# Kernel optimization log

Measured on AMD Instinct MI355X. Metric: run time of the kernel, lower is better.

Reference implementation:

```python
import jax, jax.numpy as jnp
import numpy as np

NUM_HEADS = 16

def setup_inputs() -> dict:
    key = jax.random.key(0)
    ks = jax.random.split(key, 8)
    T, B, E = 2048, 2, 1024
    s = 1.0 / np.sqrt(E)
    return {
        "query": jax.random.normal(ks[0], (T, B, E), jnp.float32),
        "key": jax.random.normal(ks[1], (T, B, E), jnp.float32),
        "value": jax.random.normal(ks[2], (T, B, E), jnp.float32),
        "Wq": jax.random.normal(ks[3], (E, E), jnp.float32) * s,
        "bq": jnp.zeros((E,), jnp.float32),
        "Wk": jax.random.normal(ks[4], (E, E), jnp.float32) * s,
        "bk": jnp.zeros((E,), jnp.float32),
        "Wv": jax.random.normal(ks[5], (E, E), jnp.float32) * s,
        "bv": jnp.zeros((E,), jnp.float32),
        "Wo": jax.random.normal(ks[6], (E, E), jnp.float32) * s,
        "bo": jnp.zeros((E,), jnp.float32),
    }

def reference(query, key, value, Wq, bq, Wk, bk, Wv, bv, Wo, bo):
    T, B, E = query.shape
    S = key.shape[0]
    H = NUM_HEADS
    hd = E // H
    scaling = float(hd) ** -0.5
    # linear projections (torch Linear: x @ W.T + b)
    q = (query @ Wq.T + bq).reshape(T, B, H, hd)
    k = (key @ Wk.T + bk).reshape(S, B, H, hd)
    v = (value @ Wv.T + bv).reshape(S, B, H, hd)
    # scores: (B, H, T, S)
    scores = jnp.einsum('tbhd,sbhd->bhts', q, k) * scaling
    attn = jax.nn.softmax(scores, axis=-1)  # dropout p=0
    # weighted sum: (T, B, H, hd) -> (T, B, E)
    out = jnp.einsum('bhts,sbhd->tbhd', attn, v).reshape(T, B, E)
    out = out @ Wo.T + bo
    # averaged attention weights over heads: (B, T, S)
    avg_w = attn.mean(axis=1)
    return (out, avg_w)
```

## Files before the change

kernel.cpp:

```cpp
#include <hip/hip_runtime.h>
#include <hip/hip_bf16.h>
#include <stdint.h>

#define HN 16
#define TT 2048
#define BBATCH 2
#define EE 1024
#define HD 64
#define MM 4096

#define SCALEQ 0.18033688011112042f

typedef __attribute__((ext_vector_type(8))) __bf16 bfrag;
typedef __attribute__((ext_vector_type(4))) float f32x4;

struct alignas(8) B4 { __bf16 a0, a1, a2, a3; };

__device__ __forceinline__ void gll16(const void* g, void* lds) {
  __builtin_amdgcn_global_load_lds(
      (const __attribute__((address_space(1))) void*)g,
      (__attribute__((address_space(3))) void*)lds, 16, 0, 0);
}

__device__ __forceinline__ f32x4 mfma_bf16(bfrag a, bfrag b, f32x4 c) {
  return __builtin_amdgcn_mfma_f32_16x16x32_bf16(a, b, c, 0, 0, 0);
}

__device__ __forceinline__ const bfrag* fragp(const __bf16* base, int row, int e) {
  return (const bfrag*)(base + row * 64 + ((((e >> 3) ^ row) & 7) << 3));
}
__device__ __forceinline__ void stage8(const __bf16* grow0, int gstride,
                                       __bf16* tile, int r0, int lane) {
  const int rr = lane >> 3;
  const int cl = (lane & 7) ^ rr;
  gll16(grow0 + (size_t)(r0 + rr) * gstride + cl * 8, tile + r0 * 64);
}

__device__ __forceinline__ void barrier_fence() {
  __builtin_amdgcn_s_barrier();
  __builtin_amdgcn_sched_barrier(0);
}

struct CvtArgs {
  const float* src[7];
  __bf16* dst[7];
  int n4[7];
};

__global__ __launch_bounds__(256) void cvt_all(CvtArgs a) {
  const int z = blockIdx.z;
  const int i = blockIdx.x * 256 + threadIdx.x;
  if (i < a.n4[z]) {
    float4 v = ((const float4*)a.src[z])[i];
    B4 o = {(__bf16)v.x, (__bf16)v.y, (__bf16)v.z, (__bf16)v.w};
    ((B4*)a.dst[z])[i] = o;
  }
}

template <int MT>
__device__ __forceinline__ void gemm2(const __bf16* __restrict__ X,
                                      const __bf16* __restrict__ W,
                                      const float* __restrict__ bias,
                                      void* __restrict__ out, int mode,
                                      float scale, int m0, int n0,
                                      __bf16* As0, __bf16* As1,
                                      __bf16* Bs0, __bf16* Bs1) {
  const int tid = threadIdx.x, lane = tid & 63, w = tid >> 6;
  const int wm = w >> 1, wn = w & 1;
  const int quad = lane >> 4, l16 = lane & 15;
  constexpr int FM = MT / 32;

  auto stageAB = [&](int buf, int k0) {
    __bf16* A = buf ? As1 : As0;
    __bf16* B = buf ? Bs1 : Bs0;
    #pragma unroll
    for (int c = 0; c < FM; ++c)
      stage8(X + (size_t)m0 * EE + k0, EE, A, w * (MT / 4) + c * 8, lane);
    #pragma unroll
    for (int c = 0; c < 4; ++c)
      stage8(W + (size_t)n0 * EE + k0, EE, B, w * 32 + c * 8, lane);
  };

  stageAB(0, 0);

  f32x4 acc[FM][4] = {};

  for (int it = 0; it < EE / 64; ++it) {
    const int cur = it & 1;
    __syncthreads();
    if (it + 1 < EE / 64) stageAB(1 - cur, (it + 1) * 64);

    const __bf16* A = cur ? As1 : As0;
    const __bf16* B = cur ? Bs1 : Bs0;
    #pragma unroll
    for (int ks = 0; ks < 2; ++ks) {
      bfrag a[FM], b[4];
      #pragma unroll
      for (int f = 0; f < FM; ++f)
        a[f] = *fragp(A, wm * (MT / 2) + f * 16 + l16, ks * 32 + quad * 8);
      #pragma unroll
      for (int f = 0; f < 4; ++f)
        b[f] = *fragp(B, wn * 64 + f * 16 + l16, ks * 32 + quad * 8);
      #pragma unroll
      for (int fm = 0; fm < FM; ++fm)
        #pragma unroll
        for (int fn = 0; fn < 4; ++fn)
          acc[fm][fn] = mfma_bf16(a[fm], b[fn], acc[fm][fn]);
    }
  }

  float bv[4];
  #pragma unroll
  for (int fn = 0; fn < 4; ++fn) bv[fn] = bias[n0 + wn * 64 + fn * 16 + l16];

  #pragma unroll
  for (int fm = 0; fm < FM; ++fm) {
    #pragma unroll
    for (int r = 0; r < 4; ++r) {
      const int gm = m0 + wm * (MT / 2) + fm * 16 + quad * 4 + r;
      #pragma unroll
      for (int fn = 0; fn < 4; ++fn) {
        const int gn = n0 + wn * 64 + fn * 16 + l16;
        const float v = (acc[fm][fn][r] + bv[fn]) * scale;
        if (mode == 0) {
          const int t = gm >> 1, bb = gm & 1, h = gn >> 6, d = gn & 63;
          ((__bf16*)out)[(((size_t)(bb * HN + h)) * TT + t) * HD + d] = (__bf16)v;
        } else if (mode == 2) {
          const int s = gm >> 1, bb = gm & 1, h = gn >> 6, d = gn & 63;
          ((__bf16*)out)[(((size_t)(bb * HN + h)) * HD + d) * TT + s] = (__bf16)v;
        } else {
          ((float*)out)[(size_t)gm * EE + gn] = v;
        }
      }
    }
  }
}

__global__ __launch_bounds__(256, 2) void gemm_qkv(
    const __bf16* __restrict__ xq, const __bf16* __restrict__ xk,
    const __bf16* __restrict__ xv, const __bf16* __restrict__ wq,
    const __bf16* __restrict__ wk, const __bf16* __restrict__ wv,
    const float* __restrict__ bq, const float* __restrict__ bk,
    const float* __restrict__ bv, __bf16* __restrict__ qo,
    __bf16* __restrict__ ko, __bf16* __restrict__ vo) {
  __shared__ __bf16 As[2][128 * 64];
  __shared__ __bf16 Bs[2][128 * 64];
  const int bx = blockIdx.x;
  const int m = bx & 31, n = (bx >> 5) & 7, z = bx >> 8;
  const __bf16 *X, *W;
  const float* bias;
  __bf16* out;
  int mode;
  float scale;
  if (z == 0)      { X = xq; W = wq; bias = bq; out = qo; mode = 0; scale = SCALEQ; }
  else if (z == 1) { X = xk; W = wk; bias = bk; out = ko; mode = 0; scale = 1.0f; }
  else             { X = xv; W = wv; bias = bv; out = vo; mode = 2; scale = 1.0f; }
  gemm2<128>(X, W, bias, out, mode, scale, m * 128, n * 128,
             As[0], As[1], Bs[0], Bs[1]);
}

__global__ __launch_bounds__(256, 2) void attn_fwd(const __bf16* __restrict__ qb,
                                                   const __bf16* __restrict__ kb,
                                                   const __bf16* __restrict__ vtb,
                                                   __bf16* __restrict__ ob,
                                                   float* __restrict__ linv_ws) {
  union Sh {
    __bf16 kv[2][2][2][64 * 64];
    float om[2][64 * 64];
  };
  __shared__ Sh sm;
  __shared__ float Lsum[2][128];
  __shared__ float LinvS[128];

  const int tid = threadIdx.x, lane = tid & 63, w = tid >> 6;
  const int p = w >> 1, tw = w & 1;
  const int quad = lane >> 4, l16 = lane & 15;

  const int bx = blockIdx.x;
  const int xcd = bx & 7, slot = bx >> 3;
  const int bhi = xcd * 4 + (slot >> 4);
  const int t0 = (slot & 15) * 128;
  const int b = bhi >> 4, h = bhi & 15;
  const size_t bh = (size_t)(b * HN + h);

  const __bf16* qbase = qb + (bh * TT + t0) * HD;
  const __bf16* kbase = kb + bh * TT * HD;
  const __bf16* vbase = vtb + bh * HD * TT;
  const int sBase = p * 1024;

  const int rr = lane >> 3, cs = lane & 7;
  uint4 vv[4];
  auto loadV = [&](int s1) {
    #pragma unroll
    for (int c = 0; c < 4; ++c)
      vv[c] = *(const uint4*)(vbase + s1 + (size_t)(tw * 32 + c * 8 + rr) * TT + cs * 8);
  };
  const int c0 = ((cs >= 4) ? 4 : 0) + ((2 * cs) & 3);
  const int c1 = ((cs >= 4) ? 4 : 0) + ((2 * cs + 1) & 3);
  const int h4 = ((cs >> 1) & 1) * 4;
  auto writeV = [&](__bf16* Vb) {
    #pragma unroll
    for (int c = 0; c < 4; ++c) {
      const int r = tw * 32 + c * 8 + rr;
      __bf16* rowp = Vb + r * 64;
      uint2 a; a.x = vv[c].x; a.y = vv[c].y;
      uint2 d; d.x = vv[c].z; d.y = vv[c].w;
      *(uint2*)(rowp + ((c0 ^ rr) << 3) + h4) = a;
      *(uint2*)(rowp + ((c1 ^ rr) << 3) + h4) = d;
    }
  };

  bfrag qf[4][2];
  #pragma unroll
  for (int fn = 0; fn < 4; ++fn)
    #pragma unroll
    for (int ks = 0; ks < 2; ++ks)
      qf[fn][ks] = *(const bfrag*)(qbase +
          (size_t)(tw * 64 + fn * 16 + l16) * HD + ks * 32 + quad * 8);
  __builtin_amdgcn_sched_barrier(0);

  loadV(sBase);
  #pragma unroll
  for (int c = 0; c < 4; ++c)
    stage8(kbase + (size_t)sBase * HD, HD, sm.kv[p][0][0], tw * 32 + c * 8, lane);
  asm volatile("s_waitcnt vmcnt(4)" ::: "memory");
  __builtin_amdgcn_sched_barrier(0);
  writeV(sm.kv[p][1][0]);

  bfrag ones;
  {
    union { short s[8]; bfrag v; } u;
    #pragma unroll
    for (int i = 0; i < 8; ++i) u.s[i] = 0x3F80;
    ones = u.v;
  }

  f32x4 oacc[4][4] = {};
  f32x4 lacc[4] = {};

  for (int it = 0; it < 16; ++it) {
    const int cur = it & 1;
    barrier_fence();
    if (it + 1 < 16) {
      const int s1 = sBase + (it + 1) * 64;
      loadV(s1);
      #pragma unroll
      for (int c = 0; c < 4; ++c)
        stage8(kbase + (size_t)s1 * HD, HD, sm.kv[p][0][1 - cur], tw * 32 + c * 8, lane);
      asm volatile("s_waitcnt vmcnt(4)" ::: "memory");
      __builtin_amdgcn_sched_barrier(0);
      writeV(sm.kv[p][1][1 - cur]);
      asm volatile("s_waitcnt lgkmcnt(0)" ::: "memory");
      __builtin_amdgcn_sched_barrier(0);
    } else {
      asm volatile("s_waitcnt vmcnt(0)" ::: "memory");
    }
    barrier_fence();

    f32x4 sacc[4][4] = {};
    #pragma unroll
    for (int ks = 0; ks < 2; ++ks) {
      bfrag kf[4];
      #pragma unroll
      for (int fm = 0; fm < 4; ++fm)
        kf[fm] = *fragp(sm.kv[p][0][cur], fm * 16 + l16, ks * 32 + quad * 8);
      __builtin_amdgcn_s_setprio(1);
      #pragma unroll
      for (int fm = 0; fm < 4; ++fm)
        #pragma unroll
        for (int fn = 0; fn < 4; ++fn)
          sacc[fm][fn] = mfma_bf16(kf[fm], qf[fn][ks], sacc[fm][fn]);
      __builtin_amdgcn_s_setprio(0);
    }

    union PB { __bf16 hh[8]; bfrag v; } pb[2][4];
    #pragma unroll
    for (int fm = 0; fm < 4; ++fm)
      #pragma unroll
      for (int fn = 0; fn < 4; ++fn) {
        const float p0 = __builtin_amdgcn_exp2f(sacc[fm][fn][0]);
        const float p1 = __builtin_amdgcn_exp2f(sacc[fm][fn][1]);
        const float p2 = __builtin_amdgcn_exp2f(sacc[fm][fn][2]);
        const float p3 = __builtin_amdgcn_exp2f(sacc[fm][fn][3]);
        const int hb = (fm & 1) * 4;
        pb[fm >> 1][fn].hh[hb + 0] = (__bf16)p0;
        pb[fm >> 1][fn].hh[hb + 1] = (__bf16)p1;
        pb[fm >> 1][fn].hh[hb + 2] = (__bf16)p2;
        pb[fm >> 1][fn].hh[hb + 3] = (__bf16)p3;
      }

    #pragma unroll
    for (int ks = 0; ks < 2; ++ks) {
      bfrag vf[4];
      #pragma unroll
      for (int fm = 0; fm < 4; ++fm)
        vf[fm] = *fragp(sm.kv[p][1][cur], fm * 16 + l16, ks * 32 + quad * 8);
      __builtin_amdgcn_s_setprio(1);
      #pragma unroll
      for (int fn = 0; fn < 4; ++fn)
        lacc[fn] = mfma_bf16(ones, pb[ks][fn].v, lacc[fn]);
      #pragma unroll
      for (int fm = 0; fm < 4; ++fm)
        #pragma unroll
        for (int fn = 0; fn < 4; ++fn)
          oacc[fm][fn] = mfma_bf16(vf[fm], pb[ks][fn].v, oacc[fm][fn]);
      __builtin_amdgcn_s_setprio(0);
    }
  }

  if (quad == 0)
    #pragma unroll
    for (int fn = 0; fn < 4; ++fn)
      Lsum[p][tw * 64 + fn * 16 + l16] = lacc[fn][0];

  __syncthreads();

  if (p == 1) {
    #pragma unroll
    for (int fm = 0; fm < 4; ++fm)
      #pragma unroll
      for (int fn = 0; fn < 4; ++fn)
        #pragma unroll
        for (int r = 0; r < 4; ++r)
          sm.om[tw][(fm * 16 + quad * 4 + r) * 64 + fn * 16 + l16] = oacc[fm][fn][r];
  }
  if (tid < 128) {
    const float linv = 1.0f / (Lsum[0][tid] + Lsum[1][tid]);
    LinvS[tid] = linv;
    linv_ws[bh * TT + t0 + tid] = linv;
  }
  __syncthreads();

  if (p == 0) {
    float li[4];
    #pragma unroll
    for (int fn = 0; fn < 4; ++fn) li[fn] = LinvS[tw * 64 + fn * 16 + l16];
    #pragma unroll
    for (int fm = 0; fm < 4; ++fm)
      #pragma unroll
      for (int fn = 0; fn < 4; ++fn) {
        const int t = t0 + tw * 64 + fn * 16 + l16;
        B4 o;
        __bf16* op = &o.a0;
        #pragma unroll
        for (int r = 0; r < 4; ++r) {
          const float v = (oacc[fm][fn][r] +
              sm.om[tw][(fm * 16 + quad * 4 + r) * 64 + fn * 16 + l16]) * li[fn];
          op[r] = (__bf16)v;
        }
        *(B4*)(ob + ((size_t)t * BBATCH + b) * EE + h * HD + fm * 16 + quad * 4) = o;
      }
  }
}

__device__ void avg_body(const __bf16* __restrict__ qb,
                         const __bf16* __restrict__ kb,
                         const float* __restrict__ linv_ws,
                         float* __restrict__ avg_out, int bx,
                         __bf16* Qs0, __bf16* Qs1,
                         __bf16* Ks0, __bf16* Ks1) {
  const int tid = threadIdx.x, lane = tid & 63, w = tid >> 6;
  const int wm = w >> 1, wn = w & 1;
  const int quad = lane >> 4, l16 = lane & 15;

  const int xcd = bx & 7, slot = bx >> 3;
  const int bti = xcd * 4 + (slot >> 4);
  const int s0 = (slot & 15) * 128;
  const int b = bti >> 4, t0 = (bti & 15) * 128;

  const __bf16* qt = qb + (((size_t)b * HN) * TT + t0) * HD;
  const __bf16* kt = kb + (((size_t)b * HN) * TT + s0) * HD;
  const float* lrow0 = linv_ws + ((size_t)b * HN) * TT + t0 + wm * 64;

  #pragma unroll
  for (int c = 0; c < 4; ++c) {
    stage8(qt, HD, Qs0, w * 32 + c * 8, lane);
    stage8(kt, HD, Ks0, w * 32 + c * 8, lane);
  }

  f32x4 aacc[4][4] = {};

  for (int h = 0; h < HN; ++h) {
    const int cur = h & 1;
    barrier_fence();
    if (h + 1 < HN) {
      const __bf16* qn = qt + (size_t)(h + 1) * TT * HD;
      const __bf16* kn = kt + (size_t)(h + 1) * TT * HD;
      __bf16* Qn = cur ? Qs0 : Qs1;
      __bf16* Kn = cur ? Ks0 : Ks1;
      #pragma unroll
      for (int c = 0; c < 4; ++c) {
        stage8(qn, HD, Qn, w * 32 + c * 8, lane);
        stage8(kn, HD, Kn, w * 32 + c * 8, lane);
      }
      asm volatile("s_waitcnt vmcnt(8)" ::: "memory");
    } else {
      asm volatile("s_waitcnt vmcnt(0)" ::: "memory");
    }
    barrier_fence();

    const __bf16* Qc = cur ? Qs1 : Qs0;
    const __bf16* Kc = cur ? Ks1 : Ks0;
    f32x4 sacc[4][4] = {};
    #pragma unroll
    for (int ks = 0; ks < 2; ++ks) {
      bfrag qf4[4], kf4[4];
      #pragma unroll
      for (int f = 0; f < 4; ++f)
        qf4[f] = *fragp(Qc, wm * 64 + f * 16 + l16, ks * 32 + quad * 8);
      #pragma unroll
      for (int f = 0; f < 4; ++f)
        kf4[f] = *fragp(Kc, wn * 64 + f * 16 + l16, ks * 32 + quad * 8);
      #pragma unroll
      for (int fm = 0; fm < 4; ++fm)
        #pragma unroll
        for (int fn = 0; fn < 4; ++fn)
          sacc[fm][fn] = mfma_bf16(qf4[fm], kf4[fn], sacc[fm][fn]);
    }

    const float* lr = lrow0 + (size_t)h * TT;
    f32x4 lvv[4];
    #pragma unroll
    for (int fm = 0; fm < 4; ++fm)
      lvv[fm] = *(const f32x4*)(lr + fm * 16 + quad * 4);

    #pragma unroll
    for (int fm = 0; fm < 4; ++fm)
      #pragma unroll
      for (int fn = 0; fn < 4; ++fn)
        #pragma unroll
        for (int r = 0; r < 4; ++r)
          aacc[fm][fn][r] += __builtin_amdgcn_exp2f(sacc[fm][fn][r]) * lvv[fm][r];
  }

  const float invh = 1.0f / (float)HN;
  #pragma unroll
  for (int fm = 0; fm < 4; ++fm)
    #pragma unroll
    for (int r = 0; r < 4; ++r) {
      const int t = t0 + wm * 64 + fm * 16 + quad * 4 + r;
      #pragma unroll
      for (int fn = 0; fn < 4; ++fn) {
        const int s = s0 + wn * 64 + fn * 16 + l16;
        avg_out[((size_t)b * TT + t) * TT + s] = aacc[fm][fn][r] * invh;
      }
    }
}

struct TailAvg { __bf16 Qs[2][128 * 64]; __bf16 Ks[2][128 * 64]; };
struct TailGo  { __bf16 As[2][64 * 64];  __bf16 Bs[2][128 * 64]; };
union TailSh { TailAvg a; TailGo g; };

__global__ __launch_bounds__(256, 2) void tail_fused(
    const __bf16* __restrict__ qb, const __bf16* __restrict__ kb,
    const float* __restrict__ linv_ws, float* __restrict__ avg_out,
    const __bf16* __restrict__ ob, const __bf16* __restrict__ wo,
    const float* __restrict__ bo, float* __restrict__ out) {
  __shared__ TailSh sh;
  const int bx = blockIdx.x;
  if (bx < 512) {
    avg_body(qb, kb, linv_ws, avg_out, bx,
             sh.a.Qs[0], sh.a.Qs[1], sh.a.Ks[0], sh.a.Ks[1]);
  } else {
    const int b2 = bx - 512;
    const int m = b2 & 63, n = b2 >> 6;
    gemm2<64>(ob, wo, bo, out, 3, 1.0f, m * 64, n * 128,
              sh.g.As[0], sh.g.As[1], sh.g.Bs[0], sh.g.Bs[1]);
  }
}

extern "C" void kernel_launch(void* const* d_in, const int* in_sizes, int n_in,
                              void* d_out, int out_size, void* d_ws, size_t ws_size,
                              hipStream_t stream) {
  (void)in_sizes; (void)n_in; (void)out_size; (void)ws_size;
  const float* query = (const float*)d_in[0];
  const float* key   = (const float*)d_in[1];
  const float* value = (const float*)d_in[2];
  const float* Wq = (const float*)d_in[3];
  const float* bq = (const float*)d_in[4];
  const float* Wk = (const float*)d_in[5];
  const float* bk = (const float*)d_in[6];
  const float* Wv = (const float*)d_in[7];
  const float* bv = (const float*)d_in[8];
  const float* Wo = (const float*)d_in[9];
  const float* bo = (const float*)d_in[10];

  char* ws = (char*)d_ws;
  size_t off = 0;
  auto wsalloc = [&](size_t bytes) -> void* {
    void* p = ws + off;
    off += (bytes + 255) & ~(size_t)255;
    return p;
  };
  const size_t XE = (size_t)MM * EE;
  const size_t WE = (size_t)EE * EE;
  __bf16* xq   = (__bf16*)wsalloc(XE * 2);
  __bf16* xk   = (__bf16*)wsalloc(XE * 2);
  __bf16* xv   = (__bf16*)wsalloc(XE * 2);
  __bf16* wqb  = (__bf16*)wsalloc(WE * 2);
  __bf16* wkb  = (__bf16*)wsalloc(WE * 2);
  __bf16* wvb  = (__bf16*)wsalloc(WE * 2);
  __bf16* wob  = (__bf16*)wsalloc(WE * 2);
  __bf16* qbuf = (__bf16*)wsalloc(XE * 2);
  __bf16* kbuf = (__bf16*)wsalloc(XE * 2);
  __bf16* vtbuf= (__bf16*)wsalloc(XE * 2);
  __bf16* obuf = (__bf16*)wsalloc(XE * 2);
  float* linv  = (float*)wsalloc((size_t)BBATCH * HN * TT * 4);

  CvtArgs ca;
  ca.src[0] = query; ca.dst[0] = xq;  ca.n4[0] = (int)(XE / 4);
  ca.src[1] = key;   ca.dst[1] = xk;  ca.n4[1] = (int)(XE / 4);
  ca.src[2] = value; ca.dst[2] = xv;  ca.n4[2] = (int)(XE / 4);
  ca.src[3] = Wq;    ca.dst[3] = wqb; ca.n4[3] = (int)(WE / 4);
  ca.src[4] = Wk;    ca.dst[4] = wkb; ca.n4[4] = (int)(WE / 4);
  ca.src[5] = Wv;    ca.dst[5] = wvb; ca.n4[5] = (int)(WE / 4);
  ca.src[6] = Wo;    ca.dst[6] = wob; ca.n4[6] = (int)(WE / 4);
  cvt_all<<<dim3(4096, 1, 7), 256, 0, stream>>>(ca);

  gemm_qkv<<<dim3(768), 256, 0, stream>>>(xq, xk, xv, wqb, wkb, wvb,
                                          bq, bk, bv, qbuf, kbuf, vtbuf);

  attn_fwd<<<dim3(512), 256, 0, stream>>>(qbuf, kbuf, vtbuf, obuf, linv);

  float* avg_out = (float*)d_out + (size_t)TT * BBATCH * EE;
  tail_fused<<<dim3(1024), 256, 0, stream>>>(qbuf, kbuf, linv, avg_out,
                                             obuf, wob, bo, (float*)d_out);
}
```

Before: 241.3 us.

## Restructure attention to 64-query tiles with full-KV loop per warp

The attention kernel moves from 128-query blocks, where KV is split across two warp pairs and combined through shared memory, to 64-query blocks where each of the 4 warps owns 16 queries and walks the whole KV sequence. This drops the cross-warp reduction and its extra shared memory and syncs, halves per-thread accumulators, and doubles the grid with launch bounds raised to 4 blocks per CU. In exchange, K/V tiles are loaded twice as many times overall and each MFMA step has less reuse of the loaded K/V fragments.

```diff
diff --git a/kernel.cpp b/kernel.cpp
--- a/kernel.cpp
+++ b/kernel.cpp
@@ -159,49 +159,41 @@
              As[0], As[1], Bs[0], Bs[1]);
 }
 
-__global__ __launch_bounds__(256, 2) void attn_fwd(const __bf16* __restrict__ qb,
+__global__ __launch_bounds__(256, 4) void attn_fwd(const __bf16* __restrict__ qb,
                                                    const __bf16* __restrict__ kb,
                                                    const __bf16* __restrict__ vtb,
                                                    __bf16* __restrict__ ob,
                                                    float* __restrict__ linv_ws) {
-  union Sh {
-    __bf16 kv[2][2][2][64 * 64];
-    float om[2][64 * 64];
-  };
-  __shared__ Sh sm;
-  __shared__ float Lsum[2][128];
-  __shared__ float LinvS[128];
+  __shared__ __bf16 kv[2][2][64 * 64];
 
   const int tid = threadIdx.x, lane = tid & 63, w = tid >> 6;
-  const int p = w >> 1, tw = w & 1;
   const int quad = lane >> 4, l16 = lane & 15;
 
   const int bx = blockIdx.x;
   const int xcd = bx & 7, slot = bx >> 3;
-  const int bhi = xcd * 4 + (slot >> 4);
-  const int t0 = (slot & 15) * 128;
+  const int bhi = xcd * 4 + (slot >> 5);
+  const int t0 = (slot & 31) * 64;
   const int b = bhi >> 4, h = bhi & 15;
   const size_t bh = (size_t)(b * HN + h);
 
   const __bf16* qbase = qb + (bh * TT + t0) * HD;
   const __bf16* kbase = kb + bh * TT * HD;
   const __bf16* vbase = vtb + bh * HD * TT;
-  const int sBase = p * 1024;
 
   const int rr = lane >> 3, cs = lane & 7;
-  uint4 vv[4];
+  uint4 vv[2];
   auto loadV = [&](int s1) {
     #pragma unroll
-    for (int c = 0; c < 4; ++c)
-      vv[c] = *(const uint4*)(vbase + s1 + (size_t)(tw * 32 + c * 8 + rr) * TT + cs * 8);
+    for (int c = 0; c < 2; ++c)
+      vv[c] = *(const uint4*)(vbase + s1 + (size_t)(w * 16 + c * 8 + rr) * TT + cs * 8);
   };
   const int c0 = ((cs >= 4) ? 4 : 0) + ((2 * cs) & 3);
   const int c1 = ((cs >= 4) ? 4 : 0) + ((2 * cs + 1) & 3);
   const int h4 = ((cs >> 1) & 1) * 4;
   auto writeV = [&](__bf16* Vb) {
     #pragma unroll
-    for (int c = 0; c < 4; ++c) {
-      const int r = tw * 32 + c * 8 + rr;
+    for (int c = 0; c < 2; ++c) {
+      const int r = w * 16 + c * 8 + rr;
       __bf16* rowp = Vb + r * 64;
       uint2 a; a.x = vv[c].x; a.y = vv[c].y;
       uint2 d; d.x = vv[c].z; d.y = vv[c].w;
@@ -209,23 +201,24 @@
       *(uint2*)(rowp + ((c1 ^ rr) << 3) + h4) = d;
     }
   };
-
-  bfrag qf[4][2];
-  #pragma unroll
-  for (int fn = 0; fn < 4; ++fn)
-    #pragma unroll
-    for (int ks = 0; ks < 2; ++ks)
-      qf[fn][ks] = *(const bfrag*)(qbase +
-          (size_t)(tw * 64 + fn * 16 + l16) * HD + ks * 32 + quad * 8);
+  auto stageK = [&](int s1, __bf16* Kb) {
+    #pragma unroll
+    for (int c = 0; c < 2; ++c)
+      stage8(kbase + (size_t)s1 * HD, HD, Kb, w * 16 + c * 8, lane);
+  };
+
+  bfrag qf[2];
+  #pragma unroll
+  for (int ks = 0; ks < 2; ++ks)
+    qf[ks] = *(const bfrag*)(qbase +
+        (size_t)(w * 16 + l16) * HD + ks * 32 + quad * 8);
   __builtin_amdgcn_sched_barrier(0);
 
-  loadV(sBase);
-  #pragma unroll
-  for (int c = 0; c < 4; ++c)
-    stage8(kbase + (size_t)sBase * HD, HD, sm.kv[p][0][0], tw * 32 + c * 8, lane);
-  asm volatile("s_waitcnt vmcnt(4)" ::: "memory");
+  loadV(0);
+  stageK(0, kv[0][0]);
+  asm volatile("s_waitcnt vmcnt(2)" ::: "memory");
   __builtin_amdgcn_sched_barrier(0);
-  writeV(sm.kv[p][1][0]);
+  writeV(kv[1][0]);
 
   bfrag ones;
   {
@@ -235,21 +228,19 @@
     ones = u.v;
   }
 
-  f32x4 oacc[4][4] = {};
-  f32x4 lacc[4] = {};
-
-  for (int it = 0; it < 16; ++it) {
+  f32x4 oacc[4] = {};
+  f32x4 lacc = {};
+
+  for (int it = 0; it < 32; ++it) {
     const int cur = it & 1;
     barrier_fence();
-    if (it + 1 < 16) {
-      const int s1 = sBase + (it + 1) * 64;
+    if (it + 1 < 32) {
+      const int s1 = (it + 1) * 64;
       loadV(s1);
-      #pragma unroll
-      for (int c = 0; c < 4; ++c)
-        stage8(kbase + (size_t)s1 * HD, HD, sm.kv[p][0][1 - cur], tw * 32 + c * 8, lane);
-      asm volatile("s_waitcnt vmcnt(4)" ::: "memory");
+      stageK(s1, kv[0][1 - cur]);
+      asm volatile("s_waitcnt vmcnt(2)" ::: "memory");
       __builtin_amdgcn_sched_barrier(0);
-      writeV(sm.kv[p][1][1 - cur]);
+      writeV(kv[1][1 - cur]);
       asm volatile("s_waitcnt lgkmcnt(0)" ::: "memory");
       __builtin_amdgcn_sched_barrier(0);
     } else {
@@ -257,99 +248,59 @@
     }
     barrier_fence();
 
-    f32x4 sacc[4][4] = {};
+    f32x4 sacc[4] = {};
     #pragma unroll
     for (int ks = 0; ks < 2; ++ks) {
       bfrag kf[4];
       #pragma unroll
       for (int fm = 0; fm < 4; ++fm)
-        kf[fm] = *fragp(sm.kv[p][0][cur], fm * 16 + l16, ks * 32 + quad * 8);
+        kf[fm] = *fragp(kv[0][cur], fm * 16 + l16, ks * 32 + quad * 8);
       __builtin_amdgcn_s_setprio(1);
       #pragma unroll
       for (int fm = 0; fm < 4; ++fm)
-        #pragma unroll
-        for (int fn = 0; fn < 4; ++fn)
-          sacc[fm][fn] = mfma_bf16(kf[fm], qf[fn][ks], sacc[fm][fn]);
+        sacc[fm] = mfma_bf16(kf[fm], qf[ks], sacc[fm]);
       __builtin_amdgcn_s_setprio(0);
     }
 
-    union PB { __bf16 hh[8]; bfrag v; } pb[2][4];
-    #pragma unroll
-    for (int fm = 0; fm < 4; ++fm)
-      #pragma unroll
-      for (int fn = 0; fn < 4; ++fn) {
-        const float p0 = __builtin_amdgcn_exp2f(sacc[fm][fn][0]);
-        const float p1 = __builtin_amdgcn_exp2f(sacc[fm][fn][1]);
-        const float p2 = __builtin_amdgcn_exp2f(sacc[fm][fn][2]);
-        const float p3 = __builtin_amdgcn_exp2f(sacc[fm][fn][3]);
-        const int hb = (fm & 1) * 4;
-        pb[fm >> 1][fn].hh[hb + 0] = (__bf16)p0;
-        pb[fm >> 1][fn].hh[hb + 1] = (__bf16)p1;
-        pb[fm >> 1][fn].hh[hb + 2] = (__bf16)p2;
-        pb[fm >> 1][fn].hh[hb + 3] = (__bf16)p3;
-      }
+    union PB { __bf16 hh[8]; bfrag v; } pb[2];
+    #pragma unroll
+    for (int fm = 0; fm < 4; ++fm) {
+      const float p0 = __builtin_amdgcn_exp2f(sacc[fm][0]);
+      const float p1 = __builtin_amdgcn_exp2f(sacc[fm][1]);
+      const float p2 = __builtin_amdgcn_exp2f(sacc[fm][2]);
+      const float p3 = __builtin_amdgcn_exp2f(sacc[fm][3]);
+      const int hb = (fm & 1) * 4;
+      pb[fm >> 1].hh[hb + 0] = (__bf16)p0;
+      pb[fm >> 1].hh[hb + 1] = (__bf16)p1;
+      pb[fm >> 1].hh[hb + 2] = (__bf16)p2;
+      pb[fm >> 1].hh[hb + 3] = (__bf16)p3;
+    }
 
     #pragma unroll
     for (int ks = 0; ks < 2; ++ks) {
       bfrag vf[4];
       #pragma unroll
       for (int fm = 0; fm < 4; ++fm)
-        vf[fm] = *fragp(sm.kv[p][1][cur], fm * 16 + l16, ks * 32 + quad * 8);
+        vf[fm] = *fragp(kv[1][cur], fm * 16 + l16, ks * 32 + quad * 8);
       __builtin_amdgcn_s_setprio(1);
-      #pragma unroll
-      for (int fn = 0; fn < 4; ++fn)
-        lacc[fn] = mfma_bf16(ones, pb[ks][fn].v, lacc[fn]);
+      lacc = mfma_bf16(ones, pb[ks].v, lacc);
       #pragma unroll
       for (int fm = 0; fm < 4; ++fm)
-        #pragma unroll
-        for (int fn = 0; fn < 4; ++fn)
-          oacc[fm][fn] = mfma_bf16(vf[fm], pb[ks][fn].v, oacc[fm][fn]);
+        oacc[fm] = mfma_bf16(vf[fm], pb[ks].v, oacc[fm]);
       __builtin_amdgcn_s_setprio(0);
     }
   }
 
-  if (quad == 0)
-    #pragma unroll
-    for (int fn = 0; fn < 4; ++fn)
-      Lsum[p][tw * 64 + fn * 16 + l16] = lacc[fn][0];
-
-  __syncthreads();
-
-  if (p == 1) {
-    #pragma unroll
-    for (int fm = 0; fm < 4; ++fm)
-      #pragma unroll
-      for (int fn = 0; fn < 4; ++fn)
-        #pragma unroll
-        for (int r = 0; r < 4; ++r)
-          sm.om[tw][(fm * 16 + quad * 4 + r) * 64 + fn * 16 + l16] = oacc[fm][fn][r];
-  }
-  if (tid < 128) {
-    const float linv = 1.0f / (Lsum[0][tid] + Lsum[1][tid]);
-    LinvS[tid] = linv;
-    linv_ws[bh * TT + t0 + tid] = linv;
-  }
-  __syncthreads();
-
-  if (p == 0) {
-    float li[4];
-    #pragma unroll
-    for (int fn = 0; fn < 4; ++fn) li[fn] = LinvS[tw * 64 + fn * 16 + l16];
-    #pragma unroll
-    for (int fm = 0; fm < 4; ++fm)
-      #pragma unroll
-      for (int fn = 0; fn < 4; ++fn) {
-        const int t = t0 + tw * 64 + fn * 16 + l16;
-        B4 o;
-        __bf16* op = &o.a0;
-        #pragma unroll
-        for (int r = 0; r < 4; ++r) {
-          const float v = (oacc[fm][fn][r] +
-              sm.om[tw][(fm * 16 + quad * 4 + r) * 64 + fn * 16 + l16]) * li[fn];
-          op[r] = (__bf16)v;
-        }
-        *(B4*)(ob + ((size_t)t * BBATCH + b) * EE + h * HD + fm * 16 + quad * 4) = o;
-      }
+  const int t = t0 + w * 16 + l16;
+  const float linv = 1.0f / lacc[0];
+  if (quad == 0) linv_ws[bh * TT + t] = linv;
+  #pragma unroll
+  for (int fm = 0; fm < 4; ++fm) {
+    B4 o;
+    __bf16* op = &o.a0;
+    #pragma unroll
+    for (int r = 0; r < 4; ++r) op[r] = (__bf16)(oacc[fm][r] * linv);
+    *(B4*)(ob + ((size_t)t * BBATCH + b) * EE + h * HD + fm * 16 + quad * 4) = o;
   }
 }
 
@@ -520,7 +471,7 @@
   gemm_qkv<<<dim3(768), 256, 0, stream>>>(xq, xk, xv, wqb, wkb, wvb,
                                           bq, bk, bv, qbuf, kbuf, vtbuf);
 
-  attn_fwd<<<dim3(512), 256, 0, stream>>>(qbuf, kbuf, vtbuf, obuf, linv);
+  attn_fwd<<<dim3(1024), 256, 0, stream>>>(qbuf, kbuf, vtbuf, obuf, linv);
 
   float* avg_out = (float*)d_out + (size_t)TT * BBATCH * EE;
   tail_fused<<<dim3(1024), 256, 0, stream>>>(qbuf, kbuf, linv, avg_out,
```

Measured after the change: 246.5 us. +2.2%, slower.
